# Kernel tuning notes

Hardware: AMD Instinct MI355X
Metric: run time of the kernel (lower is better)

## Reference

```python
import jax, jax.numpy as jnp
import numpy as np

EMBED_DICT = 200
EMBED_DIM = 16
HIDDEN = 32
LSTM_DIM = 256
B, C, L = 8192, 16, 64
END_IDX = 1  # stand-in for token_list.index('<End>')


def _lin(k, i, o):
    return jax.random.normal(k, (i, o), jnp.float32) * (1.0 / np.sqrt(i))


def setup_inputs() -> dict:
    key = jax.random.key(0)
    ks = jax.random.split(key, 20)
    feat_in = EMBED_DIM * 14 + LSTM_DIM  # 480
    z = lambda n: jnp.zeros((n,), jnp.float32)
    return {
        "trees": jax.random.randint(ks[0], (B, 1 + C, 17), 0, L),
        "lstm_out_list": jax.random.normal(ks[1], (B, L, 1, LSTM_DIM), jnp.float32),
        "first_notes": jax.random.normal(ks[2], (B, EMBED_DIM), jnp.float32),
        "train": 1,
        "embedding": jax.random.normal(ks[3], (EMBED_DICT, EMBED_DIM), jnp.float32) * 0.05,
        "leaf_end_W": _lin(ks[4], EMBED_DIM, HIDDEN), "leaf_end_b": z(HIDDEN),
        "lc_W1": _lin(ks[5], feat_in, HIDDEN * 4), "lc_b1": z(HIDDEN * 4),
        "lc_W2": _lin(ks[6], HIDDEN * 4, HIDDEN), "lc_b2": z(HIDDEN),
        "cs_W1": _lin(ks[7], HIDDEN * 2, HIDDEN * 4), "cs_b1": z(HIDDEN * 4),
        "cs_W2": _lin(ks[8], HIDDEN * 4, HIDDEN), "cs_b2": z(HIDDEN),
        "nf_W1": _lin(ks[9], feat_in, HIDDEN * 4), "nf_b1": z(HIDDEN * 4),
        "nf_W2": _lin(ks[10], HIDDEN * 4, HIDDEN), "nf_b2": z(HIDDEN),
        "cb_W1": _lin(ks[11], HIDDEN * 2, HIDDEN * 4), "cb_b1": z(HIDDEN * 4),
        "cb_W2": _lin(ks[12], HIDDEN * 4, HIDDEN), "cb_b2": z(HIDDEN),
        "ff_W1": _lin(ks[13], HIDDEN, HIDDEN), "ff_b1": z(HIDDEN),
        "ff_W2": _lin(ks[14], HIDDEN, HIDDEN), "ff_b2": z(HIDDEN),
        "ts_W": _lin(ks[15], HIDDEN, 1), "ts_b": z(1),
    }


def _mlp2(x, W1, b1, W2, b2):
    # Linear -> ReLU -> Linear -> ReLU (matches nn.Sequential blocks)
    return jax.nn.relu(jax.nn.relu(x @ W1 + b1) @ W2 + b2)


def reference(trees, lstm_out_list, first_notes, train, embedding,
              leaf_end_W, leaf_end_b, lc_W1, lc_b1, lc_W2, lc_b2,
              cs_W1, cs_b1, cs_W2, cs_b2, nf_W1, nf_b1, nf_W2, nf_b2,
              cb_W1, cb_b1, cb_W2, cb_b2, ff_W1, ff_b1, ff_W2, ff_b2,
              ts_W, ts_b):
    Bn = trees.shape[0]
    root = trees[:, 0, :]        # (B, 17)
    leaves = trees[:, 1:, :]     # (B, C, 17)
    Cn = leaves.shape[1]
    bidx = jnp.arange(Bn)

    # ---- leaf nodes: either leaf_end_ff(embed(type)) or leaf_child_ff(concat) ----
    leaf_tok = embedding[leaves[:, :, 2:-1]].reshape(Bn, Cn, -1)       # (B,C,224)
    leaf_ptr = lstm_out_list[bidx[:, None], leaves[:, :, -1], 0, :]    # (B,C,256)
    leaf_child = _mlp2(jnp.concatenate([leaf_tok, leaf_ptr], -1),
                       lc_W1, lc_b1, lc_W2, lc_b2)                     # (B,C,32)
    leaf_end = embedding[leaves[:, :, 2]] @ leaf_end_W + leaf_end_b    # (B,C,32)
    is_end = (leaves[:, :, 2] == END_IDX)[..., None]
    children = jnp.where(is_end, leaf_end, leaf_child)                 # (B,C,32)

    # ---- sequential left fold with child_sum_ff over children ----
    def step(carry, child):
        nxt = _mlp2(jnp.concatenate([carry, child], -1), cs_W1, cs_b1, cs_W2, cs_b2)
        return nxt, None
    child_summary, _ = jax.lax.scan(step, children[:, 0],
                                    jnp.moveaxis(children[:, 1:], 0, 1))  # (B,32)

    # ---- root node embedding + combine ----
    node_tok = embedding[root[:, 2:-1]].reshape(Bn, -1)                # (B,224)
    node_ptr = lstm_out_list[bidx, root[:, -1], 0, :]                  # (B,256)
    node_tmp = _mlp2(jnp.concatenate([node_tok, node_ptr], -1),
                     nf_W1, nf_b1, nf_W2, nf_b2)                       # (B,32)
    tree_sum = _mlp2(jnp.concatenate([node_tmp, child_summary], -1),
                     cb_W1, cb_b1, cb_W2, cb_b2)                       # (B,32)

    # ---- head: two linears (no activation) then score ----
    ff = (tree_sum @ ff_W1 + ff_b1) @ ff_W2 + ff_b2
    return ff @ ts_W + ts_b                                            # (B,1)
```

## Files before the change

### kernel.cpp

```cpp
#include <hip/hip_runtime.h>
#include <cstddef>


typedef __bf16 bf16x8 __attribute__((ext_vector_type(8)));
typedef __bf16 bf16x4 __attribute__((ext_vector_type(4)));
typedef float  f32x4  __attribute__((ext_vector_type(4)));

__global__ __launch_bounds__(256) void prep_kernel(
    const float* __restrict__ embedding,
    const float* __restrict__ leaf_end_W, const float* __restrict__ leaf_end_b,
    const float* __restrict__ lc_W1, const float* __restrict__ lc_W2,
    const float* __restrict__ nf_W1, const float* __restrict__ nf_W2,
    const float* __restrict__ cs_W1, const float* __restrict__ cs_W2,
    const float* __restrict__ cb_W1, const float* __restrict__ cb_W2,
    const float* __restrict__ ff_W1, const float* __restrict__ ff_b1,
    const float* __restrict__ ff_W2, const float* __restrict__ ff_b2,
    const float* __restrict__ ts_W, const float* __restrict__ ts_b,
    __bf16* __restrict__ lcW1T, __bf16* __restrict__ nfW1T,
    __bf16* __restrict__ lcW2T, __bf16* __restrict__ nfW2T,
    __bf16* __restrict__ emb_bf, float* __restrict__ endvec,
    __bf16* __restrict__ csW1Th, __bf16* __restrict__ csW1Tl,
    __bf16* __restrict__ cbW1Th, __bf16* __restrict__ cbW1Tl,
    __bf16* __restrict__ csW2Th, __bf16* __restrict__ csW2Tl,
    __bf16* __restrict__ cbW2Th, __bf16* __restrict__ cbW2Tl,
    float* __restrict__ vfin, float* __restrict__ cfin)
{
    const int id = blockIdx.x * 256 + threadIdx.x;
    if (id < 61440) {
        const int k = id >> 7, n = id & 127;
        lcW1T[n * 480 + k] = (__bf16)lc_W1[id];
    } else if (id < 122880) {
        const int e = id - 61440;
        const int k = e >> 7, n = e & 127;
        nfW1T[n * 480 + k] = (__bf16)nf_W1[e];
    } else if (id < 126976) {
        const int e = id - 122880;
        const int k = e >> 5, n = e & 31;
        lcW2T[n * 128 + k] = (__bf16)lc_W2[e];
    } else if (id < 131072) {
        const int e = id - 126976;
        const int k = e >> 5, n = e & 31;
        nfW2T[n * 128 + k] = (__bf16)nf_W2[e];
    } else if (id < 134272) {
        emb_bf[id - 131072] = (__bf16)embedding[id - 131072];
    } else if (id < 134304) {
        const int c = id - 134272;
        float a = leaf_end_b[c];
        #pragma unroll
        for (int d = 0; d < 16; ++d) a = fmaf(embedding[16 + d], leaf_end_W[d * 32 + c], a);
        endvec[c] = a;
    } else if (id < 142496) {
        const int e = id - 134304;
        const int k = e >> 7, n = e & 127;
        const float v = cs_W1[e];
        const __bf16 h = (__bf16)v;
        csW1Th[n * 64 + k] = h; csW1Tl[n * 64 + k] = (__bf16)(v - (float)h);
    } else if (id < 150688) {
        const int e = id - 142496;
        const int k = e >> 7, n = e & 127;
        const float v = cb_W1[e];
        const __bf16 h = (__bf16)v;
        cbW1Th[n * 64 + k] = h; cbW1Tl[n * 64 + k] = (__bf16)(v - (float)h);
    } else if (id < 154784) {
        const int e = id - 150688;
        const int k = e >> 5, n = e & 31;
        const float v = cs_W2[e];
        const __bf16 h = (__bf16)v;
        csW2Th[n * 128 + k] = h; csW2Tl[n * 128 + k] = (__bf16)(v - (float)h);
    } else if (id < 158880) {
        const int e = id - 154784;
        const int k = e >> 5, n = e & 31;
        const float v = cb_W2[e];
        const __bf16 h = (__bf16)v;
        cbW2Th[n * 128 + k] = h; cbW2Tl[n * 128 + k] = (__bf16)(v - (float)h);
    } else if (id < 158912) {
        const int c = id - 158880;
        float w2t[32];
        #pragma unroll
        for (int k = 0; k < 32; ++k) {
            float a = 0.f;
            for (int j = 0; j < 32; ++j) a = fmaf(ff_W2[k * 32 + j], ts_W[j], a);
            w2t[k] = a;
        }
        float a = 0.f;
        #pragma unroll
        for (int k = 0; k < 32; ++k) a = fmaf(ff_W1[c * 32 + k], w2t[k], a);
        vfin[c] = a;
    } else if (id == 158912) {
        float a = ts_b[0];
        for (int j = 0; j < 32; ++j) a = fmaf(ff_b2[j], ts_W[j], a);
        for (int k = 0; k < 32; ++k) {
            float w2t = 0.f;
            for (int j = 0; j < 32; ++j) w2t = fmaf(ff_W2[k * 32 + j], ts_W[j], w2t);
            a = fmaf(ff_b1[k], w2t, a);
        }
        cfin[0] = a;
    }
}

__global__ __launch_bounds__(256, 6) void mlp1_mfma(
    const int* __restrict__ trees,
    const float* __restrict__ lstm,
    const __bf16* __restrict__ lcW1T, const __bf16* __restrict__ nfW1T,
    const __bf16* __restrict__ lcW2T, const __bf16* __restrict__ nfW2T,
    const __bf16* __restrict__ emb_bf, const float* __restrict__ endvec,
    const float* __restrict__ lc_b1, const float* __restrict__ lc_b2,
    const float* __restrict__ nf_b1, const float* __restrict__ nf_b2,
    __bf16* __restrict__ childrenH, __bf16* __restrict__ childrenL,
    __bf16* __restrict__ node_tmpH, __bf16* __restrict__ node_tmpL)
{
    __shared__ __align__(16) __bf16 emb_s[3200];
    __shared__ __align__(16) __bf16 Hs[32][136];
    __shared__ float b1s[128], b2s[32], evs[32];
    __shared__ int   endf[32];

    const int tid = threadIdx.x;
    const int blk = blockIdx.x;
    const bool leaf = (blk < 4096);

    const __bf16* __restrict__ W1T = leaf ? lcW1T : nfW1T;
    const __bf16* __restrict__ W2T = leaf ? lcW2T : nfW2T;
    const float*  __restrict__ b1p = leaf ? lc_b1 : nf_b1;
    const float*  __restrict__ b2p = leaf ? lc_b2 : nf_b2;

    for (int i = tid; i < 3200; i += 256) emb_s[i] = emb_bf[i];
    if (tid < 128) b1s[tid] = b1p[tid];
    if (tid < 32)  { b2s[tid] = b2p[tid]; evs[tid] = leaf ? endvec[tid] : 0.f; }
    if (tid < 32) {
        if (leaf) {
            const int R = blk * 32 + tid;
            const int b = R >> 4, trow = 1 + (R & 15);
            endf[tid] = (trees[(b * 17 + trow) * 17 + 2] == 1);
        } else endf[tid] = 0;
    }

    const int l  = tid & 63;
    const int w  = tid >> 6;
    const int lm = l & 15;
    const int kb = l >> 4;
    const int rowbase = (w >> 1) * 16;
    const int colbase = (w & 1) * 64;

    const int row = rowbase + lm;
    int b, trow;
    if (leaf) { const int R = blk * 32 + row; b = R >> 4; trow = 1 + (R & 15); }
    else      { b = (blk - 4096) * 32 + row; trow = 0; }
    const int* __restrict__ ti = trees + (b * 17 + trow) * 17;
    const float* __restrict__ lrow = lstm + ((size_t)b * 64 + (size_t)ti[16]) * 256;

    f32x4 acc[4];
    #pragma unroll
    for (int j = 0; j < 4; ++j) acc[j] = (f32x4){0.f, 0.f, 0.f, 0.f};

    __syncthreads();

    #pragma unroll
    for (int c = 0; c < 15; ++c) {
        bf16x8 wfr[4];
        #pragma unroll
        for (int ct = 0; ct < 4; ++ct) {
            const int n = colbase + ct * 16 + lm;
            wfr[ct] = *(const bf16x8*)(W1T + n * 480 + c * 32 + kb * 8);
        }
        bf16x8 afr;
        if (c < 7) {
            const int tok = ti[2 + 2 * c + (kb >> 1)];
            afr = *(const bf16x8*)(emb_s + tok * 16 + (kb & 1) * 8);
        } else {
            const float* p = lrow + (c - 7) * 32 + kb * 8;
            const float4 u = *(const float4*)p;
            const float4 v = *(const float4*)(p + 4);
            bf16x8 t;
            t[0] = (__bf16)u.x; t[1] = (__bf16)u.y; t[2] = (__bf16)u.z; t[3] = (__bf16)u.w;
            t[4] = (__bf16)v.x; t[5] = (__bf16)v.y; t[6] = (__bf16)v.z; t[7] = (__bf16)v.w;
            afr = t;
        }
        #pragma unroll
        for (int ct = 0; ct < 4; ++ct)
            acc[ct] = __builtin_amdgcn_mfma_f32_16x16x32_bf16(wfr[ct], afr, acc[ct], 0, 0, 0);
    }

    #pragma unroll
    for (int ct = 0; ct < 4; ++ct) {
        const int wcol = colbase + ct * 16 + 4 * kb;
        bf16x4 pk;
        #pragma unroll
        for (int rg = 0; rg < 4; ++rg) {
            float v = acc[ct][rg] + b1s[wcol + rg];
            v = v > 0.f ? v : 0.f;
            pk[rg] = (__bf16)v;
        }
        *(bf16x4*)&Hs[rowbase + lm][wcol] = pk;
    }
    __syncthreads();

    const int mt = w >> 1, jn = w & 1;
    f32x4 a2 = (f32x4){0.f, 0.f, 0.f, 0.f};
    #pragma unroll
    for (int kc = 0; kc < 4; ++kc) {
        const bf16x8 wf = *(const bf16x8*)(W2T + (jn * 16 + lm) * 128 + kc * 32 + kb * 8);
        const bf16x8 hf = *(const bf16x8*)(&Hs[mt * 16 + lm][kc * 32 + kb * 8]);
        a2 = __builtin_amdgcn_mfma_f32_16x16x32_bf16(wf, hf, a2, 0, 0, 0);
    }

    {
        const int orow = mt * 16 + lm;
        const int ocol = jn * 16 + 4 * kb;
        const bool isend = leaf && endf[orow];
        bf16x4 ph, pl;
        #pragma unroll
        for (int rg = 0; rg < 4; ++rg) {
            float v = a2[rg] + b2s[ocol + rg];
            v = v > 0.f ? v : 0.f;
            if (isend) v = evs[ocol + rg];
            const __bf16 h = (__bf16)v;
            ph[rg] = h;
            pl[rg] = (__bf16)(v - (float)h);
        }
        if (leaf) {
            const size_t R = (size_t)blk * 32 + orow;
            *(bf16x4*)&childrenH[R * 32 + ocol] = ph;
            *(bf16x4*)&childrenL[R * 32 + ocol] = pl;
        } else {
            const size_t R = (size_t)(blk - 4096) * 32 + orow;
            *(bf16x4*)&node_tmpH[R * 32 + ocol] = ph;
            *(bf16x4*)&node_tmpL[R * 32 + ocol] = pl;
        }
    }
}

__global__ __launch_bounds__(256) void scan_mfma(
    const __bf16* __restrict__ childrenH, const __bf16* __restrict__ childrenL,
    const __bf16* __restrict__ node_tmpH, const __bf16* __restrict__ node_tmpL,
    const __bf16* __restrict__ csW1Th, const __bf16* __restrict__ csW1Tl,
    const __bf16* __restrict__ csW2Th, const __bf16* __restrict__ csW2Tl,
    const __bf16* __restrict__ cbW1Th, const __bf16* __restrict__ cbW1Tl,
    const __bf16* __restrict__ cbW2Th, const __bf16* __restrict__ cbW2Tl,
    const float* __restrict__ cs_b1, const float* __restrict__ cs_b2,
    const float* __restrict__ cb_b1, const float* __restrict__ cb_b2,
    const float* __restrict__ vfin_g, const float* __restrict__ cfin_g,
    float* __restrict__ out)
{
    __shared__ __align__(16) __bf16 Xh[32][72], Xl[32][72];
    __shared__ __align__(16) __bf16 Hh[32][136], Hl[32][136];
    __shared__ float b1a[128], b1b[128], b2a[32], b2b[32], vfin[32];
    __shared__ float psum[2][32];
    __shared__ float cfin_s;

    const int tid = threadIdx.x;
    const int l = tid & 63, w = tid >> 6;
    const int lm = l & 15, kb = l >> 4;

    if (tid < 128)      { b1a[tid] = cs_b1[tid]; b1b[tid] = cb_b1[tid]; }
    else if (tid < 160) { b2a[tid - 128] = cs_b2[tid - 128]; b2b[tid - 128] = cb_b2[tid - 128]; }
    else if (tid < 192) { vfin[tid - 160] = vfin_g[tid - 160]; }
    else if (tid == 192) cfin_s = cfin_g[0];

    bf16x8 W1r[2][2][2];
    #pragma unroll
    for (int nt = 0; nt < 2; ++nt)
        #pragma unroll
        for (int kc = 0; kc < 2; ++kc) {
            const int n = w * 32 + nt * 16 + lm;
            W1r[nt][kc][0] = *(const bf16x8*)(csW1Th + n * 64 + kc * 32 + kb * 8);
            W1r[nt][kc][1] = *(const bf16x8*)(csW1Tl + n * 64 + kc * 32 + kb * 8);
        }
    bf16x8 W2r[4][2];
    {
        const int n2 = (w & 1) * 16 + lm;
        #pragma unroll
        for (int kc = 0; kc < 4; ++kc) {
            W2r[kc][0] = *(const bf16x8*)(csW2Th + n2 * 128 + kc * 32 + kb * 8);
            W2r[kc][1] = *(const bf16x8*)(csW2Tl + n2 * 128 + kc * 32 + kb * 8);
        }
    }

    const size_t base = (size_t)blockIdx.x * 32;
    const int tt = tid >> 3, c4 = (tid & 7) * 4;

    {
        const size_t o0 = ((base + tt) * 16 + 0) * 32 + c4;
        const size_t o1 = ((base + tt) * 16 + 1) * 32 + c4;
        *(bf16x4*)&Xh[tt][c4]      = *(const bf16x4*)(childrenH + o0);
        *(bf16x4*)&Xl[tt][c4]      = *(const bf16x4*)(childrenL + o0);
        *(bf16x4*)&Xh[tt][32 + c4] = *(const bf16x4*)(childrenH + o1);
        *(bf16x4*)&Xl[tt][32 + c4] = *(const bf16x4*)(childrenL + o1);
    }
    __syncthreads();

    #pragma unroll 1
    for (int it = 1; it <= 16; ++it) {
        const bool fin = (it == 16);
        if (fin) {
            #pragma unroll
            for (int nt = 0; nt < 2; ++nt)
                #pragma unroll
                for (int kc = 0; kc < 2; ++kc) {
                    const int n = w * 32 + nt * 16 + lm;
                    W1r[nt][kc][0] = *(const bf16x8*)(cbW1Th + n * 64 + kc * 32 + kb * 8);
                    W1r[nt][kc][1] = *(const bf16x8*)(cbW1Tl + n * 64 + kc * 32 + kb * 8);
                }
            const int n2 = (w & 1) * 16 + lm;
            #pragma unroll
            for (int kc = 0; kc < 4; ++kc) {
                W2r[kc][0] = *(const bf16x8*)(cbW2Th + n2 * 128 + kc * 32 + kb * 8);
                W2r[kc][1] = *(const bf16x8*)(cbW2Tl + n2 * 128 + kc * 32 + kb * 8);
            }
        }
        const float* __restrict__ b1c = fin ? b1b : b1a;
        const float* __restrict__ b2c = fin ? b2b : b2a;

        bf16x4 pfh, pfl;
        const int pfmode = (it < 15) ? 1 : (it == 15 ? 2 : 0);
        if (pfmode == 1) {
            const size_t o = ((base + tt) * 16 + (it + 1)) * 32 + c4;
            pfh = *(const bf16x4*)(childrenH + o);
            pfl = *(const bf16x4*)(childrenL + o);
        } else if (pfmode == 2) {
            const size_t o = (base + tt) * 32 + c4;
            pfh = *(const bf16x4*)(node_tmpH + o);
            pfl = *(const bf16x4*)(node_tmpL + o);
        }

        bf16x8 xh[2][2], xl[2][2];
        #pragma unroll
        for (int tn = 0; tn < 2; ++tn)
            #pragma unroll
            for (int kc = 0; kc < 2; ++kc) {
                xh[tn][kc] = *(const bf16x8*)&Xh[tn * 16 + lm][kc * 32 + kb * 8];
                xl[tn][kc] = *(const bf16x8*)&Xl[tn * 16 + lm][kc * 32 + kb * 8];
            }
        f32x4 a1[2][2];
        #pragma unroll
        for (int tn = 0; tn < 2; ++tn)
            #pragma unroll
            for (int nt = 0; nt < 2; ++nt) {
                a1[tn][nt] = (f32x4){0.f, 0.f, 0.f, 0.f};
                #pragma unroll
                for (int kc = 0; kc < 2; ++kc) {
                    a1[tn][nt] = __builtin_amdgcn_mfma_f32_16x16x32_bf16(W1r[nt][kc][0], xh[tn][kc], a1[tn][nt], 0, 0, 0);
                    a1[tn][nt] = __builtin_amdgcn_mfma_f32_16x16x32_bf16(W1r[nt][kc][0], xl[tn][kc], a1[tn][nt], 0, 0, 0);
                    a1[tn][nt] = __builtin_amdgcn_mfma_f32_16x16x32_bf16(W1r[nt][kc][1], xh[tn][kc], a1[tn][nt], 0, 0, 0);
                }
            }
        #pragma unroll
        for (int tn = 0; tn < 2; ++tn)
            #pragma unroll
            for (int nt = 0; nt < 2; ++nt) {
                const int wcol = w * 32 + nt * 16 + 4 * kb;
                bf16x4 ph, pl;
                #pragma unroll
                for (int rg = 0; rg < 4; ++rg) {
                    float v = a1[tn][nt][rg] + b1c[wcol + rg];
                    v = v > 0.f ? v : 0.f;
                    const __bf16 h = (__bf16)v;
                    ph[rg] = h;
                    pl[rg] = (__bf16)(v - (float)h);
                }
                *(bf16x4*)&Hh[tn * 16 + lm][wcol] = ph;
                *(bf16x4*)&Hl[tn * 16 + lm][wcol] = pl;
            }
        __syncthreads();

        const int mt = w >> 1, jn = w & 1;
        f32x4 a2 = (f32x4){0.f, 0.f, 0.f, 0.f};
        #pragma unroll
        for (int kc = 0; kc < 4; ++kc) {
            const bf16x8 hh = *(const bf16x8*)&Hh[mt * 16 + lm][kc * 32 + kb * 8];
            const bf16x8 hl = *(const bf16x8*)&Hl[mt * 16 + lm][kc * 32 + kb * 8];
            a2 = __builtin_amdgcn_mfma_f32_16x16x32_bf16(W2r[kc][0], hh, a2, 0, 0, 0);
            a2 = __builtin_amdgcn_mfma_f32_16x16x32_bf16(W2r[kc][0], hl, a2, 0, 0, 0);
            a2 = __builtin_amdgcn_mfma_f32_16x16x32_bf16(W2r[kc][1], hh, a2, 0, 0, 0);
        }

        if (!fin) {
            const int cb_ = (it == 15) ? 32 : 0;
            const int ocol = jn * 16 + 4 * kb;
            bf16x4 ph, pl;
            #pragma unroll
            for (int rg = 0; rg < 4; ++rg) {
                float v = a2[rg] + b2c[ocol + rg];
                v = v > 0.f ? v : 0.f;
                const __bf16 h = (__bf16)v;
                ph[rg] = h;
                pl[rg] = (__bf16)(v - (float)h);
            }
            *(bf16x4*)&Xh[mt * 16 + lm][cb_ + ocol] = ph;
            *(bf16x4*)&Xl[mt * 16 + lm][cb_ + ocol] = pl;
            if (pfmode) {
                const int dst = (pfmode == 2) ? 0 : 32;
                *(bf16x4*)&Xh[tt][dst + c4] = pfh;
                *(bf16x4*)&Xl[tt][dst + c4] = pfl;
            }
            __syncthreads();
        } else {
            const int ocol = jn * 16 + 4 * kb;
            float p = 0.f;
            #pragma unroll
            for (int rg = 0; rg < 4; ++rg) {
                float v = a2[rg] + b2c[ocol + rg];
                v = v > 0.f ? v : 0.f;
                p = fmaf(v, vfin[ocol + rg], p);
            }
            p += __shfl_xor(p, 16, 64);
            p += __shfl_xor(p, 32, 64);
            if (kb == 0) psum[jn][mt * 16 + lm] = p;
            __syncthreads();
            if (tid < 32) out[base + tid] = cfin_s + psum[0][tid] + psum[1][tid];
        }
    }
}

extern "C" void kernel_launch(void* const* d_in, const int* in_sizes, int n_in,
                              void* d_out, int out_size, void* d_ws, size_t ws_size,
                              hipStream_t stream) {
    const int*   trees      = (const int*)d_in[0];
    const float* lstm       = (const float*)d_in[1];
    const float* embedding  = (const float*)d_in[4];
    const float* leaf_end_W = (const float*)d_in[5];
    const float* leaf_end_b = (const float*)d_in[6];
    const float* lc_W1 = (const float*)d_in[7];
    const float* lc_b1 = (const float*)d_in[8];
    const float* lc_W2 = (const float*)d_in[9];
    const float* lc_b2 = (const float*)d_in[10];
    const float* cs_W1 = (const float*)d_in[11];
    const float* cs_b1 = (const float*)d_in[12];
    const float* cs_W2 = (const float*)d_in[13];
    const float* cs_b2 = (const float*)d_in[14];
    const float* nf_W1 = (const float*)d_in[15];
    const float* nf_b1 = (const float*)d_in[16];
    const float* nf_W2 = (const float*)d_in[17];
    const float* nf_b2 = (const float*)d_in[18];
    const float* cb_W1 = (const float*)d_in[19];
    const float* cb_b1 = (const float*)d_in[20];
    const float* cb_W2 = (const float*)d_in[21];
    const float* cb_b2 = (const float*)d_in[22];
    const float* ff_W1 = (const float*)d_in[23];
    const float* ff_b1 = (const float*)d_in[24];
    const float* ff_W2 = (const float*)d_in[25];
    const float* ff_b2 = (const float*)d_in[26];
    const float* ts_W  = (const float*)d_in[27];
    const float* ts_b  = (const float*)d_in[28];

    char* ws = (char*)d_ws;
    __bf16* childrenH = (__bf16*)ws;
    __bf16* childrenL = (__bf16*)(ws + 8388608);
    __bf16* node_tmpH = (__bf16*)(ws + 16777216);
    __bf16* node_tmpL = (__bf16*)(ws + 17301504);
    __bf16* lcW1T    = (__bf16*)(ws + 17825792);
    __bf16* nfW1T    = (__bf16*)(ws + 17948672);
    __bf16* lcW2T    = (__bf16*)(ws + 18071552);
    __bf16* nfW2T    = (__bf16*)(ws + 18079744);
    __bf16* emb_bf   = (__bf16*)(ws + 18087936);
    float*  endvec   = (float*)(ws + 18094336);
    __bf16* csW1Th   = (__bf16*)(ws + 18094464);
    __bf16* csW1Tl   = (__bf16*)(ws + 18110848);
    __bf16* cbW1Th   = (__bf16*)(ws + 18127232);
    __bf16* cbW1Tl   = (__bf16*)(ws + 18143616);
    __bf16* csW2Th   = (__bf16*)(ws + 18160000);
    __bf16* csW2Tl   = (__bf16*)(ws + 18168192);
    __bf16* cbW2Th   = (__bf16*)(ws + 18176384);
    __bf16* cbW2Tl   = (__bf16*)(ws + 18184576);
    float*  vfin     = (float*)(ws + 18192768);
    float*  cfin     = (float*)(ws + 18192896);
    float*  outp     = (float*)d_out;

    prep_kernel<<<dim3(621), dim3(256), 0, stream>>>(
        embedding, leaf_end_W, leaf_end_b, lc_W1, lc_W2, nf_W1, nf_W2,
        cs_W1, cs_W2, cb_W1, cb_W2, ff_W1, ff_b1, ff_W2, ff_b2, ts_W, ts_b,
        lcW1T, nfW1T, lcW2T, nfW2T, emb_bf, endvec,
        csW1Th, csW1Tl, cbW1Th, cbW1Tl, csW2Th, csW2Tl, cbW2Th, cbW2Tl,
        vfin, cfin);

    mlp1_mfma<<<dim3(4352), dim3(256), 0, stream>>>(
        trees, lstm, lcW1T, nfW1T, lcW2T, nfW2T, emb_bf, endvec,
        lc_b1, lc_b2, nf_b1, nf_b2, childrenH, childrenL, node_tmpH, node_tmpL);

    scan_mfma<<<dim3(256), dim3(256), 0, stream>>>(
        childrenH, childrenL, node_tmpH, node_tmpL,
        csW1Th, csW1Tl, csW2Th, csW2Tl, cbW1Th, cbW1Tl, cbW2Th, cbW2Tl,
        cs_b1, cs_b2, cb_b1, cb_b2, vfin, cfin, outp);
}
```

Before: 150.0 us.

## Double rows per block in first MLP kernel and pad embedding LDS rows

Each block of the leaf/root MLP kernel now processes 64 rows instead of 32, so each wave computes two 16-row tiles and reuses the same W1 weight fragments for both. This halves the per-block overhead of staging the embedding table in LDS and halves W1 fragment reloads. The embedding table in LDS is padded to a 24-element row stride to reduce bank conflicts on token gathers. The cost is higher register pressure (launch bounds lowered to 4), fewer blocks, and larger LDS use.

```diff
diff --git a/kernel.cpp b/kernel.cpp
--- a/kernel.cpp
+++ b/kernel.cpp
@@ -98,7 +98,7 @@
     }
 }
 
-__global__ __launch_bounds__(256, 6) void mlp1_mfma(
+__global__ __launch_bounds__(256, 4) void mlp1_mfma(
     const int* __restrict__ trees,
     const float* __restrict__ lstm,
     const __bf16* __restrict__ lcW1T, const __bf16* __restrict__ nfW1T,
@@ -109,48 +109,59 @@
     __bf16* __restrict__ childrenH, __bf16* __restrict__ childrenL,
     __bf16* __restrict__ node_tmpH, __bf16* __restrict__ node_tmpL)
 {
-    __shared__ __align__(16) __bf16 emb_s[3200];
-    __shared__ __align__(16) __bf16 Hs[32][136];
+    __shared__ __align__(16) __bf16 emb_s[200 * 24];
+    __shared__ __align__(16) __bf16 Hs[64][136];
     __shared__ float b1s[128], b2s[32], evs[32];
-    __shared__ int   endf[32];
+    __shared__ int   endf[64];
 
     const int tid = threadIdx.x;
     const int blk = blockIdx.x;
-    const bool leaf = (blk < 4096);
+    const bool leaf = (blk < 2048);
 
     const __bf16* __restrict__ W1T = leaf ? lcW1T : nfW1T;
     const __bf16* __restrict__ W2T = leaf ? lcW2T : nfW2T;
     const float*  __restrict__ b1p = leaf ? lc_b1 : nf_b1;
     const float*  __restrict__ b2p = leaf ? lc_b2 : nf_b2;
 
-    for (int i = tid; i < 3200; i += 256) emb_s[i] = emb_bf[i];
-    if (tid < 128) b1s[tid] = b1p[tid];
-    if (tid < 32)  { b2s[tid] = b2p[tid]; evs[tid] = leaf ? endvec[tid] : 0.f; }
-    if (tid < 32) {
-        if (leaf) {
-            const int R = blk * 32 + tid;
-            const int b = R >> 4, trow = 1 + (R & 15);
-            endf[tid] = (trees[(b * 17 + trow) * 17 + 2] == 1);
-        } else endf[tid] = 0;
-    }
-
     const int l  = tid & 63;
     const int w  = tid >> 6;
     const int lm = l & 15;
     const int kb = l >> 4;
-    const int rowbase = (w >> 1) * 16;
-    const int colbase = (w & 1) * 64;
-
-    const int row = rowbase + lm;
-    int b, trow;
-    if (leaf) { const int R = blk * 32 + row; b = R >> 4; trow = 1 + (R & 15); }
-    else      { b = (blk - 4096) * 32 + row; trow = 0; }
-    const int* __restrict__ ti = trees + (b * 17 + trow) * 17;
-    const float* __restrict__ lrow = lstm + ((size_t)b * 64 + (size_t)ti[16]) * 256;
-
-    f32x4 acc[4];
-    #pragma unroll
-    for (int j = 0; j < 4; ++j) acc[j] = (f32x4){0.f, 0.f, 0.f, 0.f};
+    const int wm = w >> 1;
+    const int wn = w & 1;
+
+    const int* tb[2];
+    const float* lb[2];
+    #pragma unroll
+    for (int i = 0; i < 2; ++i) {
+        const int r = wm * 32 + i * 16 + lm;
+        int b, trow;
+        if (leaf) { const int R = blk * 64 + r; b = R >> 4; trow = 1 + (R & 15); }
+        else      { b = (blk - 2048) * 64 + r; trow = 0; }
+        const int* t = trees + (b * 17 + trow) * 17;
+        tb[i] = t;
+        lb[i] = lstm + ((size_t)b * 64 + (size_t)t[16]) * 256;
+    }
+
+    for (int i = tid; i < 3200; i += 256) {
+        const int row = i >> 4, col = i & 15;
+        emb_s[row * 24 + col] = emb_bf[i];
+    }
+    if (tid < 128) b1s[tid] = b1p[tid];
+    if (tid < 32)  { b2s[tid] = b2p[tid]; evs[tid] = leaf ? endvec[tid] : 0.f; }
+    if (tid < 64) {
+        if (leaf) {
+            const int R = blk * 64 + tid;
+            const int b = R >> 4, trow = 1 + (R & 15);
+            endf[tid] = (trees[(b * 17 + trow) * 17 + 2] == 1);
+        } else endf[tid] = 0;
+    }
+
+    f32x4 acc[2][4];
+    #pragma unroll
+    for (int i = 0; i < 2; ++i)
+        #pragma unroll
+        for (int j = 0; j < 4; ++j) acc[i][j] = (f32x4){0.f, 0.f, 0.f, 0.f};
 
     __syncthreads();
 
@@ -159,58 +170,75 @@
         bf16x8 wfr[4];
         #pragma unroll
         for (int ct = 0; ct < 4; ++ct) {
-            const int n = colbase + ct * 16 + lm;
+            const int n = wn * 64 + ct * 16 + lm;
             wfr[ct] = *(const bf16x8*)(W1T + n * 480 + c * 32 + kb * 8);
         }
-        bf16x8 afr;
+        bf16x8 bfr[2];
         if (c < 7) {
-            const int tok = ti[2 + 2 * c + (kb >> 1)];
-            afr = *(const bf16x8*)(emb_s + tok * 16 + (kb & 1) * 8);
+            #pragma unroll
+            for (int i = 0; i < 2; ++i) {
+                const int tok = tb[i][2 + 2 * c + (kb >> 1)];
+                bfr[i] = *(const bf16x8*)(emb_s + tok * 24 + (kb & 1) * 8);
+            }
         } else {
-            const float* p = lrow + (c - 7) * 32 + kb * 8;
-            const float4 u = *(const float4*)p;
-            const float4 v = *(const float4*)(p + 4);
-            bf16x8 t;
-            t[0] = (__bf16)u.x; t[1] = (__bf16)u.y; t[2] = (__bf16)u.z; t[3] = (__bf16)u.w;
-            t[4] = (__bf16)v.x; t[5] = (__bf16)v.y; t[6] = (__bf16)v.z; t[7] = (__bf16)v.w;
-            afr = t;
-        }
-        #pragma unroll
-        for (int ct = 0; ct < 4; ++ct)
-            acc[ct] = __builtin_amdgcn_mfma_f32_16x16x32_bf16(wfr[ct], afr, acc[ct], 0, 0, 0);
-    }
-
-    #pragma unroll
-    for (int ct = 0; ct < 4; ++ct) {
-        const int wcol = colbase + ct * 16 + 4 * kb;
-        bf16x4 pk;
-        #pragma unroll
-        for (int rg = 0; rg < 4; ++rg) {
-            float v = acc[ct][rg] + b1s[wcol + rg];
-            v = v > 0.f ? v : 0.f;
-            pk[rg] = (__bf16)v;
-        }
-        *(bf16x4*)&Hs[rowbase + lm][wcol] = pk;
-    }
+            #pragma unroll
+            for (int i = 0; i < 2; ++i) {
+                const float* p = lb[i] + (c - 7) * 32 + kb * 8;
+                const float4 u = *(const float4*)p;
+                const float4 v = *(const float4*)(p + 4);
+                bf16x8 t;
+                t[0] = (__bf16)u.x; t[1] = (__bf16)u.y; t[2] = (__bf16)u.z; t[3] = (__bf16)u.w;
+                t[4] = (__bf16)v.x; t[5] = (__bf16)v.y; t[6] = (__bf16)v.z; t[7] = (__bf16)v.w;
+                bfr[i] = t;
+            }
+        }
+        #pragma unroll
+        for (int i = 0; i < 2; ++i)
+            #pragma unroll
+            for (int ct = 0; ct < 4; ++ct)
+                acc[i][ct] = __builtin_amdgcn_mfma_f32_16x16x32_bf16(wfr[ct], bfr[i], acc[i][ct], 0, 0, 0);
+    }
+
+    #pragma unroll
+    for (int i = 0; i < 2; ++i)
+        #pragma unroll
+        for (int ct = 0; ct < 4; ++ct) {
+            const int wcol = wn * 64 + ct * 16 + 4 * kb;
+            bf16x4 pk;
+            #pragma unroll
+            for (int rg = 0; rg < 4; ++rg) {
+                float v = acc[i][ct][rg] + b1s[wcol + rg];
+                v = v > 0.f ? v : 0.f;
+                pk[rg] = (__bf16)v;
+            }
+            *(bf16x4*)&Hs[wm * 32 + i * 16 + lm][wcol] = pk;
+        }
     __syncthreads();
 
-    const int mt = w >> 1, jn = w & 1;
-    f32x4 a2 = (f32x4){0.f, 0.f, 0.f, 0.f};
+    const int jn = w & 1, rb2 = 2 * (w >> 1);
+    f32x4 acc2[2];
+    acc2[0] = (f32x4){0.f, 0.f, 0.f, 0.f};
+    acc2[1] = (f32x4){0.f, 0.f, 0.f, 0.f};
+
     #pragma unroll
     for (int kc = 0; kc < 4; ++kc) {
         const bf16x8 wf = *(const bf16x8*)(W2T + (jn * 16 + lm) * 128 + kc * 32 + kb * 8);
-        const bf16x8 hf = *(const bf16x8*)(&Hs[mt * 16 + lm][kc * 32 + kb * 8]);
-        a2 = __builtin_amdgcn_mfma_f32_16x16x32_bf16(wf, hf, a2, 0, 0, 0);
-    }
-
-    {
-        const int orow = mt * 16 + lm;
+        #pragma unroll
+        for (int i = 0; i < 2; ++i) {
+            const bf16x8 hf = *(const bf16x8*)(&Hs[(rb2 + i) * 16 + lm][kc * 32 + kb * 8]);
+            acc2[i] = __builtin_amdgcn_mfma_f32_16x16x32_bf16(wf, hf, acc2[i], 0, 0, 0);
+        }
+    }
+
+    #pragma unroll
+    for (int i = 0; i < 2; ++i) {
+        const int orow = (rb2 + i) * 16 + lm;
         const int ocol = jn * 16 + 4 * kb;
         const bool isend = leaf && endf[orow];
         bf16x4 ph, pl;
         #pragma unroll
         for (int rg = 0; rg < 4; ++rg) {
-            float v = a2[rg] + b2s[ocol + rg];
+            float v = acc2[i][rg] + b2s[ocol + rg];
             v = v > 0.f ? v : 0.f;
             if (isend) v = evs[ocol + rg];
             const __bf16 h = (__bf16)v;
@@ -218,11 +246,11 @@
             pl[rg] = (__bf16)(v - (float)h);
         }
         if (leaf) {
-            const size_t R = (size_t)blk * 32 + orow;
+            const size_t R = (size_t)blk * 64 + orow;
             *(bf16x4*)&childrenH[R * 32 + ocol] = ph;
             *(bf16x4*)&childrenL[R * 32 + ocol] = pl;
         } else {
-            const size_t R = (size_t)(blk - 4096) * 32 + orow;
+            const size_t R = (size_t)(blk - 2048) * 64 + orow;
             *(bf16x4*)&node_tmpH[R * 32 + ocol] = ph;
             *(bf16x4*)&node_tmpL[R * 32 + ocol] = pl;
         }
@@ -472,7 +500,7 @@
         csW1Th, csW1Tl, cbW1Th, cbW1Tl, csW2Th, csW2Tl, cbW2Th, cbW2Tl,
         vfin, cfin);
 
-    mlp1_mfma<<<dim3(4352), dim3(256), 0, stream>>>(
+    mlp1_mfma<<<dim3(2176), dim3(256), 0, stream>>>(
         trees, lstm, lcW1T, nfW1T, lcW2T, nfW2T, emb_bf, endvec,
         lc_b1, lc_b2, nf_b1, nf_b2, childrenH, childrenL, node_tmpH, node_tmpL);
 
```

New measurement: 122.7 us. -18.2%, faster.
